# Kernel optimization log

Hardware: AMD Instinct MI355X
Metric: run time of the kernel (lower is better)

The kernel has to match this reference:

```python
import jax, jax.numpy as jnp
import numpy as np

B, E, FC_N = 8, 65536, 2500
CONVS = [5, 16, 32, 64, 64]
EPS = 1e-5


def setup_inputs() -> dict:
    key = jax.random.key(0)
    ks = iter(jax.random.split(key, 32))
    inp = {
        'x': jax.random.normal(next(ks), (B, 5, E), dtype=jnp.float32),
        'gemm': jax.random.randint(next(ks), (B, E, 4), 0, E, dtype=jnp.int32),
        'old_verts': jax.random.normal(next(ks), (B, 642, 3), dtype=jnp.float32),
    }
    for i in range(4):
        ci, co = CONVS[i], CONVS[i + 1]
        inp[f'w{i}'] = jax.random.normal(next(ks), (co, ci, 5), dtype=jnp.float32) * 0.02
        inp[f'b{i}'] = jnp.zeros((co,), dtype=jnp.float32)
        inp[f'g{i}'] = jnp.ones((co,), dtype=jnp.float32)
        inp[f'beta{i}'] = jnp.zeros((co,), dtype=jnp.float32)
    inp['dw1'] = jax.random.normal(next(ks), (FC_N, CONVS[-1]), dtype=jnp.float32) * 0.02
    inp['db1'] = jnp.zeros((FC_N,), dtype=jnp.float32)
    inp['dw2'] = jax.random.normal(next(ks), (642 * 3, FC_N), dtype=jnp.float32) * 0.02
    inp['db2'] = jnp.zeros((642 * 3,), dtype=jnp.float32)
    return inp


def mesh_conv(x, gemm, w, b):
    # x: (B,C,E); gemm: (B,E,4) -> neighbor features (B,C,E,4)
    nb = jax.vmap(lambda xb, gb: xb[:, gb])(x, gemm)
    # MeshCNN symmetric features: [self, a+c, b+d, |a-c|, |b-d|]
    f = jnp.stack([
        x,
        nb[..., 0] + nb[..., 2],
        nb[..., 1] + nb[..., 3],
        jnp.abs(nb[..., 0] - nb[..., 2]),
        jnp.abs(nb[..., 1] - nb[..., 3]),
    ], axis=-1)  # (B,C,E,5)
    return jnp.einsum('bcek,ock->boe', f, w) + b[None, :, None]


def bn_relu(x, g, beta):
    # BatchNorm2d training-mode math over (batch, spatial) per channel
    mean = jnp.mean(x, axis=(0, 2), keepdims=True)
    var = jnp.var(x, axis=(0, 2), keepdims=True)
    return jax.nn.relu((x - mean) * jax.lax.rsqrt(var + EPS) * g[None, :, None] + beta[None, :, None])


def reference(x, gemm, old_verts,
              w0, b0, g0, beta0, w1, b1, g1, beta1,
              w2, b2, g2, beta2, w3, b3, g3, beta3,
              dw1, db1, dw2, db2):
    h = x[:, :5]
    params = [(w0, b0, g0, beta0), (w1, b1, g1, beta1),
              (w2, b2, g2, beta2), (w3, b3, g3, beta3)]
    for w, b, g, beta in params:
        h = bn_relu(mesh_conv(h, gemm, w, b), g, beta)
    pooled = jnp.mean(h, axis=2)                 # AvgPool1d(n_edges) -> (B, C)
    h1 = jax.nn.relu(pooled @ dw1.T + db1)       # dropout = identity (eval)
    out = h1 @ dw2.T + db2
    return out.reshape(-1, 642, 3) + old_verts
```

## Files before the change

kernel.cpp:

```cpp
#include <hip/hip_runtime.h>

#define E_DIM 65536
#define BE_TOTAL 524288
#define EPS_BN 1e-5f
#define NB_STATS 256

typedef unsigned int uint;
typedef unsigned short ushort;
typedef unsigned char uchar;
typedef __attribute__((ext_vector_type(8))) short short8;
typedef __attribute__((ext_vector_type(4))) float floatx4;

#define PB_FP8 ((size_t)BE_TOTAL*16)

__device__ __forceinline__ float bflo(uint u){ return __uint_as_float(u << 16); }
__device__ __forceinline__ float bfhi(uint u){ return __uint_as_float(u & 0xffff0000u); }

__device__ __forceinline__ ushort pbf1(float a){
  uint ua = __float_as_uint(a);
  return (ushort)((ua + 0x7fffu + ((ua >> 16) & 1u)) >> 16);
}
__device__ __forceinline__ uint packbf(float a, float b){
  return (uint)pbf1(a) | ((uint)pbf1(b) << 16);
}
__device__ __forceinline__ void unpack8(uint4 v, float* x){
  x[0]=bflo(v.x); x[1]=bfhi(v.x); x[2]=bflo(v.y); x[3]=bfhi(v.y);
  x[4]=bflo(v.z); x[5]=bfhi(v.z); x[6]=bflo(v.w); x[7]=bfhi(v.w);
}
__device__ __forceinline__ uint4 pack8u(const float* z){
  uint4 v;
  v.x = packbf(z[0],z[1]); v.y = packbf(z[2],z[3]);
  v.z = packbf(z[4],z[5]); v.w = packbf(z[6],z[7]);
  return v;
}

__device__ __forceinline__ uint2 pack8f8(const float* z){
  int lo = __builtin_amdgcn_cvt_pk_fp8_f32(z[0], z[1], 0,  false);
  lo     = __builtin_amdgcn_cvt_pk_fp8_f32(z[2], z[3], lo, true);
  int hi = __builtin_amdgcn_cvt_pk_fp8_f32(z[4], z[5], 0,  false);
  hi     = __builtin_amdgcn_cvt_pk_fp8_f32(z[6], z[7], hi, true);
  uint2 r; r.x = (uint)lo; r.y = (uint)hi; return r;
}
__device__ __forceinline__ void dec8f8(uint2 w, float* x){
  x[0]=__builtin_amdgcn_cvt_f32_fp8((int)w.x,0);
  x[1]=__builtin_amdgcn_cvt_f32_fp8((int)w.x,1);
  x[2]=__builtin_amdgcn_cvt_f32_fp8((int)w.x,2);
  x[3]=__builtin_amdgcn_cvt_f32_fp8((int)w.x,3);
  x[4]=__builtin_amdgcn_cvt_f32_fp8((int)w.y,0);
  x[5]=__builtin_amdgcn_cvt_f32_fp8((int)w.y,1);
  x[6]=__builtin_amdgcn_cvt_f32_fp8((int)w.y,2);
  x[7]=__builtin_amdgcn_cvt_f32_fp8((int)w.y,3);
}
__device__ __forceinline__ uchar f8byte(float v){
  return (uchar)(__builtin_amdgcn_cvt_pk_fp8_f32(v, 0.f, 0, false) & 0xff);
}

template<int CI, int CO>
__global__ void wprep(const float* __restrict__ w, ushort* __restrict__ img)
{
  constexpr int CHUNKS = CI/16;
  const int t = blockIdx.x*256 + threadIdx.x;
  if (t >= CHUNKS*3*CO*4) return;
  const int s  = t & 3;
  const int o  = (t >> 2) % CO;
  const int ck = (t >> 2) / CO;
  const int chunk = ck / 3;
  const int ks    = ck % 3;
  float z[8];
  #pragma unroll
  for (int j8=0;j8<8;j8++){
    const int j = s*8 + j8;
    const int ft = ks*2 + (j>>4);
    const int ci = chunk*16 + (j & 15);
    z[j8] = (ft < 5) ? w[((size_t)o*CI + ci)*5 + ft] : 0.f;
  }
  const int t4 = (o&3) ^ ((o>>2)&3);
  *reinterpret_cast<uint4*>(img + ((size_t)(ck*CO + o))*32 + ((s^t4)<<3)) = pack8u(z);
}

template<int CI, int CO>
__global__ void wprep8(const float* __restrict__ w, uchar* __restrict__ img)
{
  constexpr int CHUNKS = CI/16;
  const int t = blockIdx.x*256 + threadIdx.x;
  if (t >= CHUNKS*3*CO*4) return;
  const int g  = t & 3;
  const int o  = (t >> 2) % CO;
  const int ck = (t >> 2) / CO;
  const int chunk = ck / 3;
  const int ks    = ck % 3;
  float z[8];
  #pragma unroll
  for (int j8=0;j8<8;j8++){
    const int j = g*8 + j8;
    const int ft = ks*2 + (j>>4);
    const int ci = chunk*16 + (j & 15);
    z[j8] = (ft < 5) ? w[((size_t)o*CI + ci)*5 + ft] * 64.f : 0.f;
  }
  const int t4 = (o&3) ^ ((o>>2)&3);
  *reinterpret_cast<uint2*>(img + ((size_t)(ck*CO + o))*32 + ((g^t4)<<3)) = pack8f8(z);
}

template<int CI, int CO, bool IN_FP8, bool OUT_BF16LIN>
__launch_bounds__(256, 4)
__global__ void mconv_mfma(const char* __restrict__ hin,
                           const int* __restrict__ gemm,
                           const char* __restrict__ wimg,
                           const float* __restrict__ bias, float bscale,
                           const float* __restrict__ ss, float pkf,
                           char* __restrict__ hout,
                           float* __restrict__ spart)
{
  constexpr int CHUNKS = CI/16;
  constexpr int NT = CO/16;
  constexpr int AB  = IN_FP8 ? 32 : 64;
  constexpr int FBY = 3*128*AB;
  constexpr int OBB = 128*CO*(OUT_BF16LIN?2:1);
  constexpr int SBY = 4*2*CO*4;
  constexpr int SMEM = (FBY > OBB+SBY) ? FBY : (OBB+SBY);
  constexpr size_t PIN = IN_FP8 ? PB_FP8 : (size_t)BE_TOTAL*32;
  constexpr int RB = IN_FP8 ? 16 : 32;
  __shared__ char smem[SMEM];
  char* FB = smem;

  const int tid = threadIdx.x;
  const int bid = blockIdx.x;
  const int b   = bid & 7;
  const int e0  = (bid >> 3) * 128;
  const size_t bbase = (size_t)b << 16;

  const int lane = tid & 63;
  const int wv   = tid >> 6;
  const int col  = lane & 15;
  const int kg   = lane >> 4;
  const int t4c  = (col & 3) ^ ((col >> 2) & 3);

  floatx4 acc[2][NT];
  #pragma unroll
  for (int n=0;n<NT;n++){
    const float bv = bias[n*16 + col] * bscale;
    #pragma unroll
    for (int mt=0;mt<2;mt++) acc[mt][n] = (floatx4){bv,bv,bv,bv};
  }

  const int el = tid >> 1;
  const int hh = tid & 1;
  const int t4e = (el&3) ^ ((el>>2)&3);
  uint off[5];
  {
    const size_t idx = bbase + (size_t)(e0 + el);
    const int4 g4 = *reinterpret_cast<const int4*>(gemm + idx*4);
    off[0] = (uint)(idx*RB + hh*(RB/2));
    off[1] = (uint)((bbase + (size_t)(uint)g4.x)*RB + hh*(RB/2));
    off[2] = (uint)((bbase + (size_t)(uint)g4.y)*RB + hh*(RB/2));
    off[3] = (uint)((bbase + (size_t)(uint)g4.z)*RB + hh*(RB/2));
    off[4] = (uint)((bbase + (size_t)(uint)g4.w)*RB + hh*(RB/2));
  }

  for (int chunk=0; chunk<CHUNKS; ++chunk){
    if (chunk > 0) __syncthreads();

    float v[5][8];
    {
      const char* hp = hin + (size_t)chunk*PIN;
      if constexpr (IN_FP8){
        uint2 q[5];
        #pragma unroll
        for (int r=0;r<5;r++) q[r] = *reinterpret_cast<const uint2*>(hp + off[r]);
        #pragma unroll
        for (int r=0;r<5;r++) dec8f8(q[r], v[r]);
      } else {
        uint4 q[5];
        #pragma unroll
        for (int r=0;r<5;r++) q[r] = *reinterpret_cast<const uint4*>(hp + off[r]);
        #pragma unroll
        for (int r=0;r<5;r++) unpack8(q[r], v[r]);
      }
    }
    const int cb = chunk*16 + hh*8;
    #pragma unroll
    for (int c=0;c<8;c++){
      const float sc = ss[cb+c], sh = ss[CI+cb+c];
      #pragma unroll
      for (int r=0;r<5;r++) v[r][c] = fmaxf(fmaf(v[r][c], sc, sh), 0.f);
    }
    float y[5][8];
    #pragma unroll
    for (int c=0;c<8;c++){
      y[0][c] = v[0][c];
      y[1][c] = v[1][c] + v[3][c];
      y[2][c] = v[2][c] + v[4][c];
      y[3][c] = fabsf(v[1][c] - v[3][c]);
      y[4][c] = fabsf(v[2][c] - v[4][c]);
    }
    if constexpr (IN_FP8){
      #pragma unroll
      for (int ks=0; ks<3; ks++){
        char* base = FB + ks*(128*32) + el*32;
        *reinterpret_cast<uint2*>(base + (((0+hh)^t4e)<<3)) = pack8f8(y[2*ks]);
        if (ks < 2){
          *reinterpret_cast<uint2*>(base + (((2+hh)^t4e)<<3)) = pack8f8(y[2*ks+1]);
        } else {
          uint2 zz; zz.x=0u; zz.y=0u;
          *reinterpret_cast<uint2*>(base + (((2+hh)^t4e)<<3)) = zz;
        }
      }
    } else {
      #pragma unroll
      for (int ks=0; ks<3; ks++){
        char* base = FB + ks*8192 + el*64;
        *reinterpret_cast<uint4*>(base + (((0+hh)^t4e)<<4)) = pack8u(y[2*ks]);
        if (ks < 2){
          *reinterpret_cast<uint4*>(base + (((2+hh)^t4e)<<4)) = pack8u(y[2*ks+1]);
        } else {
          const uint4 zz = {0,0,0,0};
          *reinterpret_cast<uint4*>(base + (((2+hh)^t4e)<<4)) = zz;
        }
      }
    }
    __syncthreads();

    const char* WG = wimg + (size_t)chunk*(3*CO*AB);
    #pragma unroll
    for (int ks=0; ks<3; ks++){
      if constexpr (IN_FP8){
        long long bf[NT];
        #pragma unroll
        for (int n=0;n<NT;n++)
          bf[n] = *reinterpret_cast<const long long*>(WG + ks*(CO*32) + n*512 + col*32 + ((kg^t4c)<<3));
        #pragma unroll
        for (int mt=0;mt<2;mt++){
          const long long af = *reinterpret_cast<const long long*>(
              FB + ks*(128*32) + (wv*32+mt*16+col)*32 + ((kg^t4c)<<3));
          #pragma unroll
          for (int n=0;n<NT;n++)
            acc[mt][n] = __builtin_amdgcn_mfma_f32_16x16x32_fp8_fp8(af, bf[n], acc[mt][n], 0, 0, 0);
        }
      } else {
        short8 bf[NT];
        #pragma unroll
        for (int n=0;n<NT;n++)
          bf[n] = *reinterpret_cast<const short8*>(WG + ks*(CO*64) + n*1024 + col*64 + ((kg^t4c)<<4));
        #pragma unroll
        for (int mt=0;mt<2;mt++){
          const short8 af = *reinterpret_cast<const short8*>(
              FB + ks*8192 + (wv*32+mt*16+col)*64 + ((kg^t4c)<<4));
          #pragma unroll
          for (int n=0;n<NT;n++)
            acc[mt][n] = __builtin_amdgcn_mfma_f32_16x16x32_bf16(af, bf[n], acc[mt][n], 0, 0, 0);
        }
      }
    }
  }

  float sred[2*NT];
  #pragma unroll
  for (int n=0;n<NT;n++){
    float s = 0.f, q2 = 0.f;
    #pragma unroll
    for (int mt=0;mt<2;mt++){
      #pragma unroll
      for (int r=0;r<4;r++){ const float vv = acc[mt][n][r]; s += vv; q2 = fmaf(vv,vv,q2); }
    }
    s  += __shfl_xor(s,16,64);  s  += __shfl_xor(s,32,64);
    q2 += __shfl_xor(q2,16,64); q2 += __shfl_xor(q2,32,64);
    sred[n] = s; sred[NT+n] = q2;
  }

  __syncthreads();
  float* SB = reinterpret_cast<float*>(smem + OBB);
  if constexpr (OUT_BF16LIN){
    ushort* OB = reinterpret_cast<ushort*>(smem);
    #pragma unroll
    for (int mt=0; mt<2; mt++){
      const int er = wv*32 + mt*16 + 4*kg;
      #pragma unroll
      for (int n=0;n<NT;n++){
        #pragma unroll
        for (int r=0;r<4;r++)
          OB[(er+r)*CO + n*16 + col] = pbf1(acc[mt][n][r]);
      }
    }
  } else {
    uchar* OB = reinterpret_cast<uchar*>(smem);
    #pragma unroll
    for (int mt=0; mt<2; mt++){
      const int er = wv*32 + mt*16 + 4*kg;
      #pragma unroll
      for (int n=0;n<NT;n++){
        #pragma unroll
        for (int r=0;r<4;r++)
          OB[(er+r)*CO + n*16 + col] = f8byte(acc[mt][n][r] * pkf);
      }
    }
  }
  if (kg == 0){
    #pragma unroll
    for (int n=0;n<NT;n++){
      SB[wv*2*CO + n*16 + col]      = sred[n];
      SB[wv*2*CO + CO + n*16 + col] = sred[NT+n];
    }
  }
  __syncthreads();
  if constexpr (OUT_BF16LIN){
    const uint4* src = reinterpret_cast<const uint4*>(smem);
    uint4* dst = reinterpret_cast<uint4*>(hout + (bbase + (size_t)e0)*CO*2);
    constexpr int NV = 128*CO/8;
    for (int i=tid; i<NV; i+=256) dst[i] = src[i];
  } else {
    constexpr int NV = 128*CO/16;
    for (int i=tid; i<NV; i+=256){
      const int pl  = i >> 7;
      const int elx = i & 127;
      const uint4 vv = *reinterpret_cast<const uint4*>(smem + elx*CO + pl*16);
      *reinterpret_cast<uint4*>(hout + (size_t)pl*PB_FP8 + (bbase + (size_t)(e0+elx))*16) = vv;
    }
  }
  if (tid < 2*CO){
    spart[(size_t)bid*2*CO + tid] =
      SB[tid] + SB[2*CO + tid] + SB[4*CO + tid] + SB[6*CO + tid];
  }
}

__launch_bounds__(256)
__global__ void conv0_kernel(const ushort* __restrict__ hin,
                             const int* __restrict__ gemm,
                             const float* __restrict__ w,
                             const float* __restrict__ bias,
                             ushort* __restrict__ hout)
{
  const int bid = blockIdx.x;
  const int swz = (bid & 7) * 256 + (bid >> 3);
  const int idx = swz * 256 + threadIdx.x;
  const int b = idx >> 16;
  const int4 g4 = *reinterpret_cast<const int4*>(gemm + (size_t)idx * 4);
  const size_t bbase = (size_t)b << 16;
  float xc[8], n0[8], n1[8], n2[8], n3[8];
  unpack8(*reinterpret_cast<const uint4*>(hin + (size_t)idx*8), xc);
  unpack8(*reinterpret_cast<const uint4*>(hin + (bbase + (size_t)(uint)g4.x)*8), n0);
  unpack8(*reinterpret_cast<const uint4*>(hin + (bbase + (size_t)(uint)g4.y)*8), n1);
  unpack8(*reinterpret_cast<const uint4*>(hin + (bbase + (size_t)(uint)g4.z)*8), n2);
  unpack8(*reinterpret_cast<const uint4*>(hin + (bbase + (size_t)(uint)g4.w)*8), n3);
  float f1[5], f2[5], f3[5], f4[5];
  #pragma unroll
  for (int c=0;c<5;c++){
    f1[c] = n0[c] + n2[c];
    f2[c] = n1[c] + n3[c];
    f3[c] = fabsf(n0[c] - n2[c]);
    f4[c] = fabsf(n1[c] - n3[c]);
  }
  float acc[16];
  #pragma unroll
  for (int o=0;o<16;o++){
    const float* wp = w + (size_t)o*25;
    float a = bias[o];
    #pragma unroll
    for (int c=0;c<5;c++){
      a = fmaf(xc[c], wp[c*5+0], a);
      a = fmaf(f1[c], wp[c*5+1], a);
      a = fmaf(f2[c], wp[c*5+2], a);
      a = fmaf(f3[c], wp[c*5+3], a);
      a = fmaf(f4[c], wp[c*5+4], a);
    }
    acc[o] = a;
  }
  #pragma unroll
  for (int o=0;o<16;o+=8){
    uint4 v;
    v.x = packbf(acc[o+0], acc[o+1]);
    v.y = packbf(acc[o+2], acc[o+3]);
    v.z = packbf(acc[o+4], acc[o+5]);
    v.w = packbf(acc[o+6], acc[o+7]);
    *reinterpret_cast<uint4*>(hout + (size_t)idx * 16 + o) = v;
  }
}

template<int CO>
__launch_bounds__(256)
__global__ void stats_kernel(const ushort* __restrict__ h, float* __restrict__ part)
{
  constexpr int GROUPS = CO / 8;
  constexpr int ROWS   = 256 / GROUPS;
  const int tid = threadIdx.x;
  const int cg  = tid % GROUPS;
  const int row = tid / GROUPS;
  float s[8], q[8];
  #pragma unroll
  for (int i=0;i<8;i++){ s[i]=0.f; q[i]=0.f; }
  for (long idx = (long)blockIdx.x*ROWS + row; idx < BE_TOTAL; idx += (long)gridDim.x*ROWS){
    uint4 v = *reinterpret_cast<const uint4*>(h + (size_t)idx*CO + cg*8);
    float x[8]; unpack8(v, x);
    #pragma unroll
    for (int i=0;i<8;i++){ s[i]+=x[i]; q[i]+=x[i]*x[i]; }
  }
  __shared__ float lds[256*16];
  #pragma unroll
  for (int i=0;i<8;i++){ lds[tid*16+i]=s[i]; lds[tid*16+8+i]=q[i]; }
  __syncthreads();
  if (tid < 2*CO){
    const int st = tid / CO;
    const int c  = tid % CO;
    const int cgg = c >> 3, ci = c & 7;
    float t = 0.f;
    for (int r=0;r<ROWS;r++) t += lds[(r*GROUPS+cgg)*16 + st*8 + ci];
    part[(size_t)blockIdx.x*(2*CO) + tid] = t;
  }
}

template<int CO>
__launch_bounds__(256)
__global__ void merge_stats(const float* __restrict__ in, float* __restrict__ out)
{
  const int t = threadIdx.x;
  if (t >= 2*CO) return;
  const int j = blockIdx.x;
  float s = 0.f;
  #pragma unroll 4
  for (int r = 0; r < 32; r++) s += in[((size_t)(j*32 + r))*(2*CO) + t];
  out[(size_t)j*(2*CO) + t] = s;
}

template<int CO>
__launch_bounds__(256)
__global__ void finalize_stats(const float* __restrict__ part, int nblk,
                               const float* __restrict__ g, const float* __restrict__ beta,
                               float invSa, float invSt, float* __restrict__ ss)
{
  constexpr int Q = 256 / CO;
  const int t = threadIdx.x;
  const int c = t % CO;
  const int qq = t / CO;
  float s = 0.f, sq = 0.f;
  for (int b = qq; b < nblk; b += Q){
    s  += part[(size_t)b*2*CO + c];
    sq += part[(size_t)b*2*CO + CO + c];
  }
  __shared__ float lsum[256], lsq[256];
  lsum[t] = s; lsq[t] = sq;
  __syncthreads();
  if (t < CO){
    float ts = 0.f, tq = 0.f;
    #pragma unroll
    for (int r = 0; r < Q; r++){ ts += lsum[r*CO + t]; tq += lsq[r*CO + t]; }
    const float inv = 1.f / (float)BE_TOTAL;
    const float mean = ts * inv * invSa;
    const float var  = tq * inv * invSa * invSa - mean*mean;
    const float scale = g[t] * rsqrtf(var + EPS_BN);
    ss[t]      = scale * invSt;
    ss[CO + t] = beta[t] - mean * scale;
  }
}

__launch_bounds__(256)
__global__ void pool_kernel(const ushort* __restrict__ h3, const float* __restrict__ ss,
                            float* __restrict__ part)
{
  const int tid = threadIdx.x;
  const int cg  = tid % 8;
  const int row = tid / 8;
  const int b   = blockIdx.x >> 6;
  const int blk = blockIdx.x & 63;
  float sc[8], sh[8];
  #pragma unroll
  for (int i=0;i<8;i++){ sc[i]=ss[cg*8+i]; sh[i]=ss[64+cg*8+i]; }
  float s[8];
  #pragma unroll
  for (int i=0;i<8;i++) s[i]=0.f;
  for (int e = blk*32 + row; e < E_DIM; e += 64*32){
    size_t idx = ((size_t)b << 16) + e;
    uint4 v = *reinterpret_cast<const uint4*>(h3 + idx*64 + cg*8);
    float x[8]; unpack8(v, x);
    #pragma unroll
    for (int i=0;i<8;i++) s[i] += fmaxf(fmaf(x[i], sc[i], sh[i]), 0.f);
  }
  __shared__ float lds[256*8];
  #pragma unroll
  for (int i=0;i<8;i++) lds[tid*8+i]=s[i];
  __syncthreads();
  if (tid < 64){
    const int c = tid, cgg = c >> 3, ci = c & 7;
    float t = 0.f;
    for (int r=0;r<32;r++) t += lds[(r*8+cgg)*8 + ci];
    part[((size_t)b*64 + blk)*64 + c] = t;
  }
}

__global__ void finalize_pool(const float* __restrict__ part, float* __restrict__ pooled)
{
  const int t = threadIdx.x;
  const int b = t >> 6, c = t & 63;
  float s = 0.f;
  for (int blk=0;blk<64;blk++) s += part[((size_t)b*64 + blk)*64 + c];
  pooled[t] = s * (1.f / (float)E_DIM);
}

__global__ void fc1_kernel(const float* __restrict__ pooled, const float* __restrict__ dw1,
                           const float* __restrict__ db1, float* __restrict__ h1t)
{
  const int n = blockIdx.x*blockDim.x + threadIdx.x;
  if (n >= 2500) return;
  float acc[8];
  const float bias = db1[n];
  #pragma unroll
  for (int b=0;b<8;b++) acc[b]=bias;
  const float* wr = dw1 + (size_t)n*64;
  #pragma unroll
  for (int c=0;c<64;c++){
    float wv = wr[c];
    #pragma unroll
    for (int b=0;b<8;b++) acc[b] = fmaf(wv, pooled[b*64+c], acc[b]);
  }
  #pragma unroll
  for (int b=0;b<8;b++) h1t[(size_t)n*8 + b] = fmaxf(acc[b], 0.f);
}

__launch_bounds__(256)
__global__ void fc2_kernel(const float* __restrict__ h1t, const float* __restrict__ dw2,
                           const float* __restrict__ db2, const float* __restrict__ oldv,
                           float* __restrict__ out)
{
  const int wv   = threadIdx.x >> 6;
  const int lane = threadIdx.x & 63;
  const int m = blockIdx.x*4 + wv;
  if (m >= 1926) return;
  const float4* wr = reinterpret_cast<const float4*>(dw2 + (size_t)m*2500);
  float acc[8];
  #pragma unroll
  for (int b=0;b<8;b++) acc[b]=0.f;
  for (int j = lane; j < 625; j += 64){
    const float4 w4 = wr[j];
    const float4* hp = reinterpret_cast<const float4*>(h1t + (size_t)j*32);
    const float4 h0a = hp[0], h0b = hp[1];
    const float4 h1a = hp[2], h1b = hp[3];
    const float4 h2a = hp[4], h2b = hp[5];
    const float4 h3a = hp[6], h3b = hp[7];
    acc[0] = fmaf(w4.x, h0a.x, fmaf(w4.y, h1a.x, fmaf(w4.z, h2a.x, fmaf(w4.w, h3a.x, acc[0]))));
    acc[1] = fmaf(w4.x, h0a.y, fmaf(w4.y, h1a.y, fmaf(w4.z, h2a.y, fmaf(w4.w, h3a.y, acc[1]))));
    acc[2] = fmaf(w4.x, h0a.z, fmaf(w4.y, h1a.z, fmaf(w4.z, h2a.z, fmaf(w4.w, h3a.z, acc[2]))));
    acc[3] = fmaf(w4.x, h0a.w, fmaf(w4.y, h1a.w, fmaf(w4.z, h2a.w, fmaf(w4.w, h3a.w, acc[3]))));
    acc[4] = fmaf(w4.x, h0b.x, fmaf(w4.y, h1b.x, fmaf(w4.z, h2b.x, fmaf(w4.w, h3b.x, acc[4]))));
    acc[5] = fmaf(w4.x, h0b.y, fmaf(w4.y, h1b.y, fmaf(w4.z, h2b.y, fmaf(w4.w, h3b.y, acc[5]))));
    acc[6] = fmaf(w4.x, h0b.z, fmaf(w4.y, h1b.z, fmaf(w4.z, h2b.z, fmaf(w4.w, h3b.z, acc[6]))));
    acc[7] = fmaf(w4.x, h0b.w, fmaf(w4.y, h1b.w, fmaf(w4.z, h2b.w, fmaf(w4.w, h3b.w, acc[7]))));
  }
  #pragma unroll
  for (int s=1; s<64; s<<=1){
    #pragma unroll
    for (int b=0;b<8;b++) acc[b] += __shfl_xor(acc[b], s, 64);
  }
  if (lane == 0){
    const float bm = db2[m];
    #pragma unroll
    for (int b=0;b<8;b++){
      const int t = b*1926 + m;
      out[t] = acc[b] + bm + oldv[t];
    }
  }
}

__launch_bounds__(256)
__global__ void transpose_x(const float* __restrict__ x, ushort* __restrict__ xt)
{
  const int idx = blockIdx.x*256 + threadIdx.x;
  const int b = idx >> 16, e = idx & 65535;
  const float* xb = x + (size_t)b*5*E_DIM + e;
  uint4 v;
  v.x = packbf(xb[0],               xb[(size_t)E_DIM]);
  v.y = packbf(xb[2*(size_t)E_DIM], xb[3*(size_t)E_DIM]);
  v.z = packbf(xb[4*(size_t)E_DIM], 0.f);
  v.w = 0u;
  *reinterpret_cast<uint4*>(xt + (size_t)idx*8) = v;
}

extern "C" void kernel_launch(void* const* d_in, const int* in_sizes, int n_in,
                              void* d_out, int out_size, void* d_ws, size_t ws_size,
                              hipStream_t stream)
{
  const float* x    = (const float*)d_in[0];
  const int*   gm   = (const int*)d_in[1];
  const float* oldv = (const float*)d_in[2];
  const float* w0 = (const float*)d_in[3],  *b0 = (const float*)d_in[4];
  const float* g0 = (const float*)d_in[5],  *be0= (const float*)d_in[6];
  const float* w1 = (const float*)d_in[7],  *b1 = (const float*)d_in[8];
  const float* g1 = (const float*)d_in[9],  *be1= (const float*)d_in[10];
  const float* w2 = (const float*)d_in[11], *b2 = (const float*)d_in[12];
  const float* g2 = (const float*)d_in[13], *be2= (const float*)d_in[14];
  const float* w3 = (const float*)d_in[15], *b3 = (const float*)d_in[16];
  const float* g3 = (const float*)d_in[17], *be3= (const float*)d_in[18];
  const float* dw1 = (const float*)d_in[19], *db1 = (const float*)d_in[20];
  const float* dw2 = (const float*)d_in[21], *db2 = (const float*)d_in[22];

  char* ws = (char*)d_ws;
  size_t off = 0;
  auto alloc = [&](size_t n){ size_t o = off; off += (n + 255) & ~(size_t)255; return o; };
  ushort* xt = (ushort*)(ws + alloc((size_t)BE_TOTAL*8*2));
  ushort* h0 = (ushort*)(ws + alloc((size_t)BE_TOTAL*16*2));
  char*   h1 = (char*)  (ws + alloc((size_t)BE_TOTAL*32));
  char*   h2 = (char*)  (ws + alloc((size_t)BE_TOTAL*64));
  ushort* h3 = (ushort*)(ws + alloc((size_t)BE_TOTAL*64*2));
  float* part   = (float*)(ws + alloc((size_t)NB_STATS*128*4));
  float* spart  = (float*)(ws + alloc((size_t)4096*128*4));
  float* mpart  = (float*)(ws + alloc((size_t)128*128*4));
  float* ss0    = (float*)(ws + alloc(512));
  float* ss1    = (float*)(ws + alloc(512));
  float* ss2    = (float*)(ws + alloc(512));
  float* ss3    = (float*)(ws + alloc(512));
  float* ppart  = (float*)(ws + alloc((size_t)8*64*64*4));
  float* pooled = (float*)(ws + alloc(512*4));
  float* h1fc   = (float*)(ws + alloc(20000*4));
  ushort* w1i   = (ushort*)(ws + alloc((size_t)3*32*32*2));
  uchar*  w2i   = (uchar*) (ws + alloc((size_t)6*64*32));
  uchar*  w3i   = (uchar*) (ws + alloc((size_t)12*64*32));
  (void)ws_size; (void)in_sizes; (void)n_in; (void)out_size;

  const int CB = BE_TOTAL/256;
  const int MB = BE_TOTAL/128;

  transpose_x<<<CB,256,0,stream>>>(x, xt);
  wprep<16,32><<<2,256,0,stream>>>(w1, w1i);
  wprep8<32,64><<<6,256,0,stream>>>(w2, w2i);
  wprep8<64,64><<<12,256,0,stream>>>(w3, w3i);

  conv0_kernel<<<CB,256,0,stream>>>(xt, gm, w0, b0, h0);
  stats_kernel<16><<<NB_STATS,256,0,stream>>>(h0, part);
  finalize_stats<16><<<1,256,0,stream>>>(part, NB_STATS, g0, be0, 1.f, 1.f, ss0);

  mconv_mfma<16,32,false,false><<<MB,256,0,stream>>>(
      (const char*)h0, gm, (const char*)w1i, b1, 1.f, ss0, 16.f, h1, spart);
  merge_stats<32><<<128,256,0,stream>>>(spart, mpart);
  finalize_stats<32><<<1,256,0,stream>>>(mpart, 128, g1, be1, 1.f, 1.f/16.f, ss1);

  mconv_mfma<32,64,true,false><<<MB,256,0,stream>>>(
      h1, gm, (const char*)w2i, b2, 64.f, ss1, 0.25f, h2, spart);
  merge_stats<64><<<128,256,0,stream>>>(spart, mpart);
  finalize_stats<64><<<1,256,0,stream>>>(mpart, 128, g2, be2, 1.f/64.f, 1.f/16.f, ss2);

  mconv_mfma<64,64,true,true><<<MB,256,0,stream>>>(
      h2, gm, (const char*)w3i, b3, 64.f, ss2, 1.f, (char*)h3, spart);
  merge_stats<64><<<128,256,0,stream>>>(spart, mpart);
  finalize_stats<64><<<1,256,0,stream>>>(mpart, 128, g3, be3, 1.f/64.f, 1.f/64.f, ss3);

  pool_kernel<<<512,256,0,stream>>>(h3, ss3, ppart);
  finalize_pool<<<1,512,0,stream>>>(ppart, pooled);
  fc1_kernel<<<10,256,0,stream>>>(pooled, dw1, db1, h1fc);
  fc2_kernel<<<482,256,0,stream>>>(h1fc, dw2, db2, oldv, (float*)d_out);
}
```

Measured before the change: 252.0 us.

## Double-buffer chunk gathers in mesh conv and store last layer as fp8

In the multi-chunk MFMA mesh-conv kernels, the gather for the next channel chunk is now issued before the current chunk's MFMAs. Features are built into two alternating LDS buffers, leaving one barrier per chunk so gather latency overlaps matrix work. Separately, the final conv layer writes its output in the fp8 chunked layout instead of bf16, and the pool kernel reads fp8, which halves that tensor's write and read traffic. The trade-offs are higher LDS use, which can lower occupancy, and extra quantisation error in the last activation.

```diff
diff --git a/kernel.cpp b/kernel.cpp
--- a/kernel.cpp
+++ b/kernel.cpp
@@ -115,9 +115,10 @@
   constexpr int NT = CO/16;
   constexpr int AB  = IN_FP8 ? 32 : 64;
   constexpr int FBY = 3*128*AB;
+  constexpr int NBUF = (CHUNKS > 1) ? 2 : 1;
   constexpr int OBB = 128*CO*(OUT_BF16LIN?2:1);
   constexpr int SBY = 4*2*CO*4;
-  constexpr int SMEM = (FBY > OBB+SBY) ? FBY : (OBB+SBY);
+  constexpr int SMEM = (NBUF*FBY > OBB+SBY) ? NBUF*FBY : (OBB+SBY);
   constexpr size_t PIN = IN_FP8 ? PB_FP8 : (size_t)BE_TOTAL*32;
   constexpr int RB = IN_FP8 ? 16 : 32;
   __shared__ char smem[SMEM];
@@ -157,26 +158,7 @@
     off[4] = (uint)((bbase + (size_t)(uint)g4.w)*RB + hh*(RB/2));
   }
 
-  for (int chunk=0; chunk<CHUNKS; ++chunk){
-    if (chunk > 0) __syncthreads();
-
-    float v[5][8];
-    {
-      const char* hp = hin + (size_t)chunk*PIN;
-      if constexpr (IN_FP8){
-        uint2 q[5];
-        #pragma unroll
-        for (int r=0;r<5;r++) q[r] = *reinterpret_cast<const uint2*>(hp + off[r]);
-        #pragma unroll
-        for (int r=0;r<5;r++) dec8f8(q[r], v[r]);
-      } else {
-        uint4 q[5];
-        #pragma unroll
-        for (int r=0;r<5;r++) q[r] = *reinterpret_cast<const uint4*>(hp + off[r]);
-        #pragma unroll
-        for (int r=0;r<5;r++) unpack8(q[r], v[r]);
-      }
-    }
+  auto BUILD = [&](float (&v)[5][8], int chunk, char* FBb){
     const int cb = chunk*16 + hh*8;
     #pragma unroll
     for (int c=0;c<8;c++){
@@ -196,7 +178,7 @@
     if constexpr (IN_FP8){
       #pragma unroll
       for (int ks=0; ks<3; ks++){
-        char* base = FB + ks*(128*32) + el*32;
+        char* base = FBb + ks*(128*32) + el*32;
         *reinterpret_cast<uint2*>(base + (((0+hh)^t4e)<<3)) = pack8f8(y[2*ks]);
         if (ks < 2){
           *reinterpret_cast<uint2*>(base + (((2+hh)^t4e)<<3)) = pack8f8(y[2*ks+1]);
@@ -208,7 +190,7 @@
     } else {
       #pragma unroll
       for (int ks=0; ks<3; ks++){
-        char* base = FB + ks*8192 + el*64;
+        char* base = FBb + ks*8192 + el*64;
         *reinterpret_cast<uint4*>(base + (((0+hh)^t4e)<<4)) = pack8u(y[2*ks]);
         if (ks < 2){
           *reinterpret_cast<uint4*>(base + (((2+hh)^t4e)<<4)) = pack8u(y[2*ks+1]);
@@ -218,8 +200,9 @@
         }
       }
     }
-    __syncthreads();
-
+  };
+
+  auto MMA = [&](int chunk, const char* FBb){
     const char* WG = wimg + (size_t)chunk*(3*CO*AB);
     #pragma unroll
     for (int ks=0; ks<3; ks++){
@@ -231,7 +214,7 @@
         #pragma unroll
         for (int mt=0;mt<2;mt++){
           const long long af = *reinterpret_cast<const long long*>(
-              FB + ks*(128*32) + (wv*32+mt*16+col)*32 + ((kg^t4c)<<3));
+              FBb + ks*(128*32) + (wv*32+mt*16+col)*32 + ((kg^t4c)<<3));
           #pragma unroll
           for (int n=0;n<NT;n++)
             acc[mt][n] = __builtin_amdgcn_mfma_f32_16x16x32_fp8_fp8(af, bf[n], acc[mt][n], 0, 0, 0);
@@ -244,11 +227,59 @@
         #pragma unroll
         for (int mt=0;mt<2;mt++){
           const short8 af = *reinterpret_cast<const short8*>(
-              FB + ks*8192 + (wv*32+mt*16+col)*64 + ((kg^t4c)<<4));
+              FBb + ks*8192 + (wv*32+mt*16+col)*64 + ((kg^t4c)<<4));
           #pragma unroll
           for (int n=0;n<NT;n++)
             acc[mt][n] = __builtin_amdgcn_mfma_f32_16x16x32_bf16(af, bf[n], acc[mt][n], 0, 0, 0);
         }
+      }
+    }
+  };
+
+  if constexpr (CHUNKS == 1){
+    float v[5][8];
+    if constexpr (IN_FP8){
+      uint2 q[5];
+      #pragma unroll
+      for (int r=0;r<5;r++) q[r] = *reinterpret_cast<const uint2*>(hin + off[r]);
+      #pragma unroll
+      for (int r=0;r<5;r++) dec8f8(q[r], v[r]);
+    } else {
+      uint4 q[5];
+      #pragma unroll
+      for (int r=0;r<5;r++) q[r] = *reinterpret_cast<const uint4*>(hin + off[r]);
+      #pragma unroll
+      for (int r=0;r<5;r++) unpack8(q[r], v[r]);
+    }
+    BUILD(v, 0, FB);
+    __syncthreads();
+    MMA(0, FB);
+  } else {
+    {
+      uint2 q[5];
+      #pragma unroll
+      for (int r=0;r<5;r++) q[r] = *reinterpret_cast<const uint2*>(hin + off[r]);
+      float v[5][8];
+      #pragma unroll
+      for (int r=0;r<5;r++) dec8f8(q[r], v[r]);
+      BUILD(v, 0, FB);
+    }
+    __syncthreads();
+    #pragma unroll
+    for (int c=0; c<CHUNKS; ++c){
+      uint2 qn[5];
+      if (c+1 < CHUNKS){
+        const char* hp = hin + (size_t)(c+1)*PIN;
+        #pragma unroll
+        for (int r=0;r<5;r++) qn[r] = *reinterpret_cast<const uint2*>(hp + off[r]);
+      }
+      MMA(c, FB + (c&1)*FBY);
+      if (c+1 < CHUNKS){
+        float v[5][8];
+        #pragma unroll
+        for (int r=0;r<5;r++) dec8f8(qn[r], v[r]);
+        BUILD(v, c+1, FB + ((c+1)&1)*FBY);
+        __syncthreads();
       }
     }
   }
@@ -452,7 +483,7 @@
 }
 
 __launch_bounds__(256)
-__global__ void pool_kernel(const ushort* __restrict__ h3, const float* __restrict__ ss,
+__global__ void pool_kernel(const char* __restrict__ h3, const float* __restrict__ ss,
                             float* __restrict__ part)
 {
   const int tid = threadIdx.x;
@@ -466,10 +497,11 @@
   float s[8];
   #pragma unroll
   for (int i=0;i<8;i++) s[i]=0.f;
+  const char* hp = h3 + (size_t)(cg>>1)*PB_FP8 + (cg&1)*8;
   for (int e = blk*32 + row; e < E_DIM; e += 64*32){
     size_t idx = ((size_t)b << 16) + e;
-    uint4 v = *reinterpret_cast<const uint4*>(h3 + idx*64 + cg*8);
-    float x[8]; unpack8(v, x);
+    uint2 v = *reinterpret_cast<const uint2*>(hp + idx*16);
+    float x[8]; dec8f8(v, x);
     #pragma unroll
     for (int i=0;i<8;i++) s[i] += fmaxf(fmaf(x[i], sc[i], sh[i]), 0.f);
   }
@@ -597,7 +629,7 @@
   ushort* h0 = (ushort*)(ws + alloc((size_t)BE_TOTAL*16*2));
   char*   h1 = (char*)  (ws + alloc((size_t)BE_TOTAL*32));
   char*   h2 = (char*)  (ws + alloc((size_t)BE_TOTAL*64));
-  ushort* h3 = (ushort*)(ws + alloc((size_t)BE_TOTAL*64*2));
+  char*   h3 = (char*)  (ws + alloc((size_t)BE_TOTAL*64));
   float* part   = (float*)(ws + alloc((size_t)NB_STATS*128*4));
   float* spart  = (float*)(ws + alloc((size_t)4096*128*4));
   float* mpart  = (float*)(ws + alloc((size_t)128*128*4));
@@ -635,10 +667,10 @@
   merge_stats<64><<<128,256,0,stream>>>(spart, mpart);
   finalize_stats<64><<<1,256,0,stream>>>(mpart, 128, g2, be2, 1.f/64.f, 1.f/16.f, ss2);
 
-  mconv_mfma<64,64,true,true><<<MB,256,0,stream>>>(
-      h2, gm, (const char*)w3i, b3, 64.f, ss2, 1.f, (char*)h3, spart);
+  mconv_mfma<64,64,true,false><<<MB,256,0,stream>>>(
+      h2, gm, (const char*)w3i, b3, 64.f, ss2, 0.25f, h3, spart);
   merge_stats<64><<<128,256,0,stream>>>(spart, mpart);
-  finalize_stats<64><<<1,256,0,stream>>>(mpart, 128, g3, be3, 1.f/64.f, 1.f/64.f, ss3);
+  finalize_stats<64><<<1,256,0,stream>>>(mpart, 128, g3, be3, 1.f/64.f, 1.f/16.f, ss3);
 
   pool_kernel<<<512,256,0,stream>>>(h3, ss3, ppart);
   finalize_pool<<<1,512,0,stream>>>(ppart, pooled);
```

After: 248.6 us. About the same (-1.4%).
